# Performance work log

Measured on AMD Instinct MI355X. Metric: run time of the kernel, lower is better.

Reference implementation:

```python
import jax, jax.numpy as jnp
import numpy as np

N, C, R, T, H, W = 2, 256, 8, 4, 32, 32
CK = C // R  # key channels = 32


def setup_inputs() -> dict:
    key = jax.random.key(0)
    ks = jax.random.split(key, 10)
    s = 0.05  # small init so dual softmax is not saturated
    return {
        "x1": jax.random.normal(ks[0], (N, C, T, H, W), jnp.float32),
        "x2": jax.random.normal(ks[1], (N, C, T, H, W), jnp.float32),
        "Wk1": jax.random.normal(ks[2], (CK, C), jnp.float32) * s,
        "bk1": jax.random.normal(ks[3], (CK,), jnp.float32) * s,
        "Wk2": jax.random.normal(ks[4], (CK, C), jnp.float32) * s,
        "bk2": jax.random.normal(ks[5], (CK,), jnp.float32) * s,
        "Wv1": jax.random.normal(ks[6], (C, C), jnp.float32) * s,
        "bv1": jax.random.normal(ks[7], (C,), jnp.float32) * s,
        "Wv2": jax.random.normal(ks[8], (C, C), jnp.float32) * s,
        "bv2": jax.random.normal(ks[9], (C,), jnp.float32) * s,
    }


def reference(x1, x2, Wk1, bk1, Wk2, bk2, Wv1, bv1, Wv2, bv2):
    n, c, t, h, w = x1.shape
    L = t * h * w
    x1f = x1.reshape(n, c, L)  # [n, C, L]
    x2f = x2.reshape(n, c, L)
    # 1x1x1 Conv3d == per-position channel mixing
    k1 = jnp.einsum('kc,ncl->nkl', Wk1, x1f) + bk1[None, :, None]  # [n, CK, L]
    k2 = jnp.einsum('kc,ncl->nkl', Wk2, x2f) + bk2[None, :, None]
    v1 = jnp.einsum('dc,ncl->ndl', Wv1, x1f) + bv1[None, :, None]  # [n, C, L]
    v2 = jnp.einsum('dc,ncl->ndl', Wv2, x2f) + bv2[None, :, None]
    # cor[n, l, m] = sum_k k1[n,k,l] * k2[n,k,m]
    cor = jnp.einsum('nkl,nkm->nlm', k1, k2)  # [n, L, L]
    attn1 = jax.nn.softmax(cor, axis=2)  # rows normalized
    attn2 = jax.nn.softmax(cor, axis=1)  # cols normalized
    r1 = jnp.einsum('ncl,nlm->ncm', v1, attn1).reshape(n, c, t, h, w)
    r2 = jnp.einsum('ncm,nlm->ncl', v2, attn2).reshape(n, c, t, h, w)
    return (x1 + r1, x2 + r2)
```

## Files before the change

### kernel.cpp

```cpp
#include <hip/hip_runtime.h>
#include <hip/hip_bf16.h>

#define N_  2
#define C_  256
#define CK_ 32
#define L_  4096

typedef __attribute__((ext_vector_type(8))) short short8;
typedef __attribute__((ext_vector_type(4))) float f32x4;
typedef __attribute__((ext_vector_type(2))) unsigned int uint2v;
typedef unsigned short ushort;

__device__ __forceinline__ ushort f2bf(float f){
  unsigned u = __float_as_uint(f);
  u += 0x7fffu + ((u >> 16) & 1u);
  return (ushort)(u >> 16);
}

__device__ __forceinline__ f32x4 mfma16(short8 a, short8 b, f32x4 c){
  return __builtin_amdgcn_mfma_f32_16x16x32_bf16(a, b, c, 0, 0, 0);
}

__global__ __launch_bounds__(256) void convert_xw_kernel(
    const float* __restrict__ x1, const float* __restrict__ x2,
    ushort* __restrict__ xT1, ushort* __restrict__ xT2,
    const float* __restrict__ Wk1, const float* __restrict__ Wk2,
    const float* __restrict__ Wv1, const float* __restrict__ Wv2,
    ushort* __restrict__ o1, ushort* __restrict__ o2,
    ushort* __restrict__ o3, ushort* __restrict__ o4){
  int b = blockIdx.x, t = threadIdx.x;
  if (b >= 512){
    int idx = (b - 512) * 256 + t;
    const int KS = CK_ * C_;
    const int VS = C_ * C_;
    if (idx < KS)                 o1[idx] = f2bf(Wk1[idx]);
    else if (idx < 2*KS)          o2[idx - KS] = f2bf(Wk2[idx - KS]);
    else if (idx < 2*KS + VS)     o3[idx - 2*KS] = f2bf(Wv1[idx - 2*KS]);
    else if (idx < 2*KS + 2*VS)   o4[idx - 2*KS - VS] = f2bf(Wv2[idx - 2*KS - VS]);
    return;
  }
  __shared__ float tt[32][264];
  int z = b & 3; int n = z & 1;
  const float* x = (z >> 1) ? x2 : x1;
  ushort* xT = (z >> 1) ? xT2 : xT1;
  int tile = b >> 2;
  int l0 = (tile & 15) * 256, c0 = (tile >> 4) * 32;
  int w = t >> 6, lam = t & 63;
  const float* xs = x + (size_t)n * C_ * L_;
  ushort* xd = xT + (size_t)n * L_ * C_;
#pragma unroll
  for (int k = 0; k < 8; ++k){
    int cr = w * 8 + k;
    float4 f = *(const float4*)(xs + (size_t)(c0 + cr) * L_ + l0 + lam * 4);
    *(float4*)&tt[cr][lam * 4] = f;
  }
  __syncthreads();
  int g = t & 3, lr = t >> 2;
#pragma unroll
  for (int k = 0; k < 4; ++k){
    int l = k * 64 + lr;
    union { __hip_bfloat162 h[4]; short8 v; } pk;
#pragma unroll
    for (int j = 0; j < 4; ++j)
      pk.h[j] = __float22bfloat162_rn(
          make_float2(tt[g*8 + 2*j][l], tt[g*8 + 2*j + 1][l]));
    *(short8*)(xd + (size_t)(l0 + l) * C_ + c0 + g * 8) = pk.v;
  }
}

#define VP_OFF(nn, cc, pp) \
  ((((size_t)(nn)*128 + ((pp)>>5))*16 + ((cc)>>4))*512 + \
   (((pp)&31)>>3)*128 + ((cc)&15)*8 + ((pp)&7))

__global__ __launch_bounds__(256) void proj_kernel(
    const ushort* __restrict__ xT1, const ushort* __restrict__ xT2,
    const ushort* __restrict__ Wk1b, const ushort* __restrict__ Wk2b,
    const ushort* __restrict__ Wv1b, const ushort* __restrict__ Wv2b,
    const float* __restrict__ bk1, const float* __restrict__ bk2,
    const float* __restrict__ bv1, const float* __restrict__ bv2,
    ushort* __restrict__ k1t, ushort* __restrict__ k2t,
    ushort* __restrict__ v1,  ushort* __restrict__ v2){
  int bid = blockIdx.x;
  int n = bid & 1, side = (bid >> 1) & 1, jh = (bid >> 2) & 1, ltile = bid >> 3;
  const ushort* X  = side ? xT2 : xT1;
  const ushort* Wv = side ? Wv2b : Wv1b;
  const ushort* Wk = side ? Wk2b : Wk1b;
  const float*  bv = side ? bv2 : bv1;
  const float*  bk = side ? bk2 : bk1;
  ushort* vout = side ? v2 : v1;
  ushort* kout = side ? k2t : k1t;
  int l0 = ltile * 64;
  int t = threadIdx.x, w = t >> 6, lane = t & 63, quad = lane >> 4, low = lane & 15;
  __shared__ ushort xs[64][264];
  const ushort* Xn = X + ((size_t)n * L_ + l0) * C_;
#pragma unroll
  for (int i = 0; i < 8; ++i){
    int flat = i * 2048 + t * 8;
    *(short8*)&xs[flat >> 8][flat & 255] = *(const short8*)(Xn + flat);
  }
  __syncthreads();
  int lw = w * 16;
  int l = l0 + lw + low;
  int njt = jh ? 5 : 4;
  for (int u = 0; u < njt; ++u){
    int jt = jh ? (4 + u) : u;
    bool isK = (jt == 8);
    const ushort* W   = isK ? Wk : Wv + (size_t)jt * 32 * C_;
    const float* bias = isK ? bk : bv + jt * 32;
    f32x4 acc0 = {}, acc1 = {};
#pragma unroll
    for (int kc = 0; kc < 8; ++kc){
      short8 b  = *(const short8*)&xs[lw + low][kc*32 + quad*8];
      short8 a0 = *(const short8*)(W + (size_t)low * C_ + kc*32 + quad*8);
      short8 a1 = *(const short8*)(W + (size_t)(16 + low) * C_ + kc*32 + quad*8);
      acc0 = mfma16(a0, b, acc0);
      acc1 = mfma16(a1, b, acc1);
    }
#pragma unroll
    for (int js = 0; js < 2; ++js){
      f32x4 acc = js ? acc1 : acc0;
      f32x4 bb = *(const f32x4*)(bias + js*16 + quad*4);
      if (!isK){
#pragma unroll
        for (int r = 0; r < 4; ++r){
          int c = jt*32 + js*16 + quad*4 + r;
          vout[VP_OFF(n, c, l)] = f2bf(acc[r] + bb[r]);
        }
      } else {
        union { ushort u4[4]; uint2v vv_; } pk;
#pragma unroll
        for (int r = 0; r < 4; ++r) pk.u4[r] = f2bf(acc[r] + bb[r]);
        *(uint2v*)(kout + ((size_t)n*L_ + l)*CK_ + js*16 + quad*4) = pk.vv_;
      }
    }
  }
}

__global__ __launch_bounds__(256) void stats_kernel(
    const ushort* __restrict__ k1t, const ushort* __restrict__ k2t,
    float* __restrict__ S1part, float* __restrict__ S2part){
  int n = blockIdx.z;
  int m0 = blockIdx.x * 128, l0 = blockIdx.y * 128;
  int t = threadIdx.x, w = t >> 6, lane = t & 63, quad = lane >> 4, low = lane & 15;
  __shared__ float rowsum[128];
  __shared__ float colsum[4][128];
  const ushort* ka = k1t + (size_t)n * L_ * CK_;
  const ushort* kb = k2t + (size_t)n * L_ * CK_;
  short8 a[2], b[8];
#pragma unroll
  for (int lt = 0; lt < 2; ++lt)
    a[lt] = *(const short8*)(ka + (size_t)(l0 + w*32 + lt*16 + low)*CK_ + quad*8);
#pragma unroll
  for (int mt = 0; mt < 8; ++mt)
    b[mt] = *(const short8*)(kb + (size_t)(m0 + mt*16 + low)*CK_ + quad*8);
  float rp[2][4] = {}; float cp[8] = {};
  const f32x4 zero = {0.f, 0.f, 0.f, 0.f};
#pragma unroll
  for (int lt = 0; lt < 2; ++lt)
#pragma unroll
    for (int mt = 0; mt < 8; ++mt){
      f32x4 e = mfma16(a[lt], b[mt], zero);
#pragma unroll
      for (int r = 0; r < 4; ++r){
        float v = __builtin_amdgcn_exp2f(e[r] * 1.44269504088896f);
        rp[lt][r] += v;
        cp[mt] += v;
      }
    }
#pragma unroll
  for (int lt = 0; lt < 2; ++lt)
#pragma unroll
    for (int r = 0; r < 4; ++r){
      float v = rp[lt][r];
      v += __shfl_xor(v, 1); v += __shfl_xor(v, 2);
      v += __shfl_xor(v, 4); v += __shfl_xor(v, 8);
      if (low == 0) rowsum[w*32 + lt*16 + quad*4 + r] = v;
    }
#pragma unroll
  for (int mt = 0; mt < 8; ++mt){
    float v = cp[mt];
    v += __shfl_xor(v, 16); v += __shfl_xor(v, 32);
    if (quad == 0) colsum[w][mt*16 + low] = v;
  }
  __syncthreads();
  if (t < 128)
    S1part[((size_t)n*32 + blockIdx.x)*L_ + l0 + t] = rowsum[t];
  else {
    int m = t - 128;
    S2part[((size_t)n*32 + blockIdx.y)*L_ + m0 + m] =
        colsum[0][m] + colsum[1][m] + colsum[2][m] + colsum[3][m];
  }
}

__global__ __launch_bounds__(256) void reduce_inv_kernel(
    const float* __restrict__ S1part, const float* __restrict__ S2part,
    float* __restrict__ invS1, float* __restrict__ invS2){
  int idx = blockIdx.x * 256 + threadIdx.x;
  int which = idx >> 13;
  int r = idx & 8191;
  int n = r >> 12, l = r & 4095;
  const float* P = which ? S2part : S1part;
  float s = 0.f;
#pragma unroll
  for (int j = 0; j < 32; ++j) s += P[((size_t)n*32 + j)*L_ + l];
  (which ? invS2 : invS1)[(size_t)n*L_ + l] = -__builtin_amdgcn_logf(s);
}

#define LOG2E_ 1.44269504088896f

__global__ __launch_bounds__(256, 2) void cross_attn_r_kernel(
    const ushort* __restrict__ k1t, const ushort* __restrict__ k2t,
    const ushort* __restrict__ v1,  const ushort* __restrict__ v2,
    const float* __restrict__ invS1, const float* __restrict__ invS2,
    const float* __restrict__ x1, const float* __restrict__ x2,
    float* __restrict__ out){
  int bid = blockIdx.x;
  int slice = bid & 7;
  int qb = bid >> 3;
  int n = slice & 1;
  int which = (slice >> 1) & 1;
  int chalf = slice >> 2;
  const ushort* kA = which ? k2t : k1t;
  const ushort* kB = which ? k1t : k2t;
  const ushort* V  = which ? v2  : v1;
  const float* iS  = which ? invS2 : invS1;
  const float* X   = which ? x2 : x1;
  float* O = out + (size_t)which * N_ * C_ * L_;
  int q0 = qb * 64, c0 = chalf * 128;
  int t = threadIdx.x, w = t >> 6, lane = t & 63, quad = lane >> 4, low = lane & 15;
  __shared__ __align__(16) float red[4][16][68];
  const ushort* kAn = kA + (size_t)n * L_ * CK_;
  const ushort* kBn = kB + (size_t)n * L_ * CK_;
  const float*  iSn = iS + (size_t)n * L_;

  const ushort* kA_base = kAn + (size_t)((low >> 2) * 8 + (low & 3)) * CK_ + quad * 8;
  const float*  sv_base = iSn + quad * 8;
  const ushort* Vp_lane = V + ((size_t)n * 128 * 16 + chalf * 8) * 512 + (size_t)lane * 8;

  short8 be[4];
#pragma unroll
  for (int qs = 0; qs < 4; ++qs)
    be[qs] = *(const short8*)(kBn + (size_t)(q0 + qs*16 + low) * CK_ + quad * 8);

  f32x4 acc[8][4] = {};
  const f32x4 zero = {0.f, 0.f, 0.f, 0.f};

  int pfirst = w * 32;
  short8 a0 = *(const short8*)(kA_base + (size_t)pfirst * CK_);
  short8 a1 = *(const short8*)(kA_base + (size_t)(pfirst + 4) * CK_);
  f32x4 sv0 = *(const f32x4*)(sv_base + pfirst);
  f32x4 sv1 = *(const f32x4*)(sv_base + pfirst + 4);

  short8 vv[8];
  {
    const ushort* vt0 = Vp_lane + (size_t)w * 16 * 512;
#pragma unroll
    for (int ct = 0; ct < 8; ++ct)
      vv[ct] = *(const short8*)(vt0 + ct * 512);
  }

#define EPH(PB, QS) do{                                                        \
    f32x4 e0 = mfma16(a0, be[QS], zero);                                       \
    f32x4 e1 = mfma16(a1, be[QS], zero);                                       \
    float p0 = __builtin_amdgcn_exp2f(__fmaf_rn(e0[0], LOG2E_, sv0[0]));       \
    float p1 = __builtin_amdgcn_exp2f(__fmaf_rn(e0[1], LOG2E_, sv0[1]));       \
    float p2 = __builtin_amdgcn_exp2f(__fmaf_rn(e0[2], LOG2E_, sv0[2]));       \
    float p3 = __builtin_amdgcn_exp2f(__fmaf_rn(e0[3], LOG2E_, sv0[3]));       \
    float p4 = __builtin_amdgcn_exp2f(__fmaf_rn(e1[0], LOG2E_, sv1[0]));       \
    float p5 = __builtin_amdgcn_exp2f(__fmaf_rn(e1[1], LOG2E_, sv1[1]));       \
    float p6 = __builtin_amdgcn_exp2f(__fmaf_rn(e1[2], LOG2E_, sv1[2]));       \
    float p7 = __builtin_amdgcn_exp2f(__fmaf_rn(e1[3], LOG2E_, sv1[3]));       \
    union { __hip_bfloat162 h[4]; short8 v; } pk;                              \
    pk.h[0] = __float22bfloat162_rn(make_float2(p0, p1));                      \
    pk.h[1] = __float22bfloat162_rn(make_float2(p2, p3));                      \
    pk.h[2] = __float22bfloat162_rn(make_float2(p4, p5));                      \
    pk.h[3] = __float22bfloat162_rn(make_float2(p6, p7));                      \
    PB = pk.v;                                                                 \
  }while(0)

  for (int kk = 0; kk < L_ / 256; ++kk){
#pragma unroll
    for (int half = 0; half < 2; ++half){
      int it = 2*kk + half;
      int itn = (it + 1) & 31;
      const ushort* vt_next = Vp_lane + (size_t)(itn*4 + w) * 16 * 512;
      int pn = itn * 128 + w * 32;
      short8 pb0, pb1;
      EPH(pb0, 0);
      EPH(pb1, 1);
      __builtin_amdgcn_s_setprio(1);
#pragma unroll
      for (int ct = 0; ct < 8; ++ct){
        acc[ct][0] = mfma16(vv[ct], pb0, acc[ct][0]);
        acc[ct][1] = mfma16(vv[ct], pb1, acc[ct][1]);
      }
      __builtin_amdgcn_s_setprio(0);
      EPH(pb0, 2);
      EPH(pb1, 3);
      a0 = *(const short8*)(kA_base + (size_t)pn * CK_);
      a1 = *(const short8*)(kA_base + (size_t)(pn + 4) * CK_);
      sv0 = *(const f32x4*)(sv_base + pn);
      sv1 = *(const f32x4*)(sv_base + pn + 4);
      __builtin_amdgcn_s_setprio(1);
#pragma unroll
      for (int ct = 0; ct < 8; ++ct){
        acc[ct][2] = mfma16(vv[ct], pb0, acc[ct][2]);
        acc[ct][3] = mfma16(vv[ct], pb1, acc[ct][3]);
        vv[ct] = *(const short8*)(vt_next + ct * 512);
      }
      __builtin_amdgcn_s_setprio(0);
    }
  }
#undef EPH

  int cl = t >> 4, qg = (t & 15) * 4;
#pragma unroll
  for (int ct = 0; ct < 8; ++ct){
#pragma unroll
    for (int qs = 0; qs < 4; ++qs)
#pragma unroll
      for (int r = 0; r < 4; ++r)
        red[w][quad*4 + r][qs*16 + low] = acc[ct][qs][r];
    __syncthreads();
    f32x4 s0 = *(const f32x4*)&red[0][cl][qg];
    f32x4 s1 = *(const f32x4*)&red[1][cl][qg];
    f32x4 s2 = *(const f32x4*)&red[2][cl][qg];
    f32x4 s3 = *(const f32x4*)&red[3][cl][qg];
    f32x4 s = (s0 + s1) + (s2 + s3);
    size_t idx = ((size_t)n * C_ + c0 + ct*16 + cl) * L_ + q0 + qg;
    const float4 xv = *(const float4*)(X + idx);
    float4 o = make_float4(xv.x + s[0], xv.y + s[1], xv.z + s[2], xv.w + s[3]);
    *(float4*)(O + idx) = o;
    __syncthreads();
  }
}

extern "C" void kernel_launch(void* const* d_in, const int* in_sizes, int n_in,
                              void* d_out, int out_size, void* d_ws, size_t ws_size,
                              hipStream_t stream) {
  const float* x1  = (const float*)d_in[0];
  const float* x2  = (const float*)d_in[1];
  const float* Wk1 = (const float*)d_in[2];
  const float* bk1 = (const float*)d_in[3];
  const float* Wk2 = (const float*)d_in[4];
  const float* bk2 = (const float*)d_in[5];
  const float* Wv1 = (const float*)d_in[6];
  const float* bv1 = (const float*)d_in[7];
  const float* Wv2 = (const float*)d_in[8];
  const float* bv2 = (const float*)d_in[9];

  char* ws = (char*)d_ws;
  size_t off = 0;
  auto carve = [&](size_t bytes) -> void* {
    void* p = ws + off; off += (bytes + 255) & ~(size_t)255; return p;
  };
  ushort* xT1   = (ushort*)carve((size_t)N_*L_*C_*2);
  ushort* xT2   = (ushort*)carve((size_t)N_*L_*C_*2);
  ushort* Wk1b  = (ushort*)carve((size_t)CK_*C_*2);
  ushort* Wk2b  = (ushort*)carve((size_t)CK_*C_*2);
  ushort* Wv1b  = (ushort*)carve((size_t)C_*C_*2);
  ushort* Wv2b  = (ushort*)carve((size_t)C_*C_*2);
  ushort* k1t   = (ushort*)carve((size_t)N_*L_*CK_*2);
  ushort* k2t   = (ushort*)carve((size_t)N_*L_*CK_*2);
  ushort* v1    = (ushort*)carve((size_t)N_*C_*L_*2);
  ushort* v2    = (ushort*)carve((size_t)N_*C_*L_*2);
  float*  S1p   = (float*)carve((size_t)N_*32*L_*4);
  float*  S2p   = (float*)carve((size_t)N_*32*L_*4);
  float*  invS1 = (float*)carve((size_t)N_*L_*4);
  float*  invS2 = (float*)carve((size_t)N_*L_*4);

  convert_xw_kernel<<<dim3(512 + (2*CK_*C_ + 2*C_*C_) / 256), 256, 0, stream>>>(
      x1, x2, xT1, xT2, Wk1, Wk2, Wv1, Wv2, Wk1b, Wk2b, Wv1b, Wv2b);
  proj_kernel<<<dim3(512), 256, 0, stream>>>(
      xT1, xT2, Wk1b, Wk2b, Wv1b, Wv2b, bk1, bk2, bv1, bv2, k1t, k2t, v1, v2);
  stats_kernel<<<dim3(L_/128, L_/128, N_), 256, 0, stream>>>(k1t, k2t, S1p, S2p);
  reduce_inv_kernel<<<dim3(2*N_*L_/256), 256, 0, stream>>>(S1p, S2p, invS1, invS2);
  cross_attn_r_kernel<<<dim3(2 * N_ * (C_/128) * (L_/64), 1, 1), 256, 0, stream>>>(
      k1t, k2t, v1, v2, invS1, invS2, x1, x2, (float*)d_out);
}
```

Before: 169.4 us.

## Fuse partial-sum reduction into stats kernel via last-block atomic counters

Removes the separate reduce_inv kernel launch. The stats kernel now bumps per-row-strip and per-column-strip atomic counters, and the last block to finish each strip sums the 32 partials and writes the negative log normaliser. The counters are zeroed in the convert kernel. The epilogue of the cross-attention kernel is also changed from float4 accesses with per-thread column groups to scalar per-lane row stores, which alters coalescing and the LDS read pattern. The cost is extra fences and atomics in every stats block.

```diff
diff --git a/kernel.cpp b/kernel.cpp
--- a/kernel.cpp
+++ b/kernel.cpp
@@ -27,10 +27,12 @@
     const float* __restrict__ Wk1, const float* __restrict__ Wk2,
     const float* __restrict__ Wv1, const float* __restrict__ Wv2,
     ushort* __restrict__ o1, ushort* __restrict__ o2,
-    ushort* __restrict__ o3, ushort* __restrict__ o4){
+    ushort* __restrict__ o3, ushort* __restrict__ o4,
+    int* __restrict__ cnts){
   int b = blockIdx.x, t = threadIdx.x;
   if (b >= 512){
     int idx = (b - 512) * 256 + t;
+    if (b == 512 && t < 128) cnts[t] = 0;
     const int KS = CK_ * C_;
     const int VS = C_ * C_;
     if (idx < KS)                 o1[idx] = f2bf(Wk1[idx]);
@@ -138,12 +140,15 @@
 
 __global__ __launch_bounds__(256) void stats_kernel(
     const ushort* __restrict__ k1t, const ushort* __restrict__ k2t,
-    float* __restrict__ S1part, float* __restrict__ S2part){
+    float* __restrict__ S1part, float* __restrict__ S2part,
+    float* __restrict__ invS1, float* __restrict__ invS2,
+    int* __restrict__ cnts){
   int n = blockIdx.z;
   int m0 = blockIdx.x * 128, l0 = blockIdx.y * 128;
   int t = threadIdx.x, w = t >> 6, lane = t & 63, quad = lane >> 4, low = lane & 15;
   __shared__ float rowsum[128];
   __shared__ float colsum[4][128];
+  __shared__ int lastv[2];
   const ushort* ka = k1t + (size_t)n * L_ * CK_;
   const ushort* kb = k2t + (size_t)n * L_ * CK_;
   short8 a[2], b[8];
@@ -190,20 +195,25 @@
     S2part[((size_t)n*32 + blockIdx.y)*L_ + m0 + m] =
         colsum[0][m] + colsum[1][m] + colsum[2][m] + colsum[3][m];
   }
-}
-
-__global__ __launch_bounds__(256) void reduce_inv_kernel(
-    const float* __restrict__ S1part, const float* __restrict__ S2part,
-    float* __restrict__ invS1, float* __restrict__ invS2){
-  int idx = blockIdx.x * 256 + threadIdx.x;
-  int which = idx >> 13;
-  int r = idx & 8191;
-  int n = r >> 12, l = r & 4095;
-  const float* P = which ? S2part : S1part;
-  float s = 0.f;
-#pragma unroll
-  for (int j = 0; j < 32; ++j) s += P[((size_t)n*32 + j)*L_ + l];
-  (which ? invS2 : invS1)[(size_t)n*L_ + l] = -__builtin_amdgcn_logf(s);
+  __threadfence();
+  if (t == 0) lastv[0] = atomicAdd(&cnts[n*32 + blockIdx.y], 1);
+  if (t == 1) lastv[1] = atomicAdd(&cnts[64 + n*32 + blockIdx.x], 1);
+  __syncthreads();
+  if (lastv[0] == 31 && t < 128){
+    __threadfence();
+    float s = 0.f;
+#pragma unroll
+    for (int j = 0; j < 32; ++j) s += S1part[((size_t)n*32 + j)*L_ + l0 + t];
+    invS1[(size_t)n*L_ + l0 + t] = -__builtin_amdgcn_logf(s);
+  }
+  if (lastv[1] == 31 && t >= 128){
+    __threadfence();
+    int m = t - 128;
+    float s = 0.f;
+#pragma unroll
+    for (int j = 0; j < 32; ++j) s += S2part[((size_t)n*32 + j)*L_ + m0 + m];
+    invS2[(size_t)n*L_ + m0 + m] = -__builtin_amdgcn_logf(s);
+  }
 }
 
 #define LOG2E_ 1.44269504088896f
@@ -313,7 +323,6 @@
   }
 #undef EPH
 
-  int cl = t >> 4, qg = (t & 15) * 4;
 #pragma unroll
   for (int ct = 0; ct < 8; ++ct){
 #pragma unroll
@@ -322,15 +331,14 @@
       for (int r = 0; r < 4; ++r)
         red[w][quad*4 + r][qs*16 + low] = acc[ct][qs][r];
     __syncthreads();
-    f32x4 s0 = *(const f32x4*)&red[0][cl][qg];
-    f32x4 s1 = *(const f32x4*)&red[1][cl][qg];
-    f32x4 s2 = *(const f32x4*)&red[2][cl][qg];
-    f32x4 s3 = *(const f32x4*)&red[3][cl][qg];
-    f32x4 s = (s0 + s1) + (s2 + s3);
-    size_t idx = ((size_t)n * C_ + c0 + ct*16 + cl) * L_ + q0 + qg;
-    const float4 xv = *(const float4*)(X + idx);
-    float4 o = make_float4(xv.x + s[0], xv.y + s[1], xv.z + s[2], xv.w + s[3]);
-    *(float4*)(O + idx) = o;
+#pragma unroll
+    for (int k = 0; k < 4; ++k){
+      int row = k * 4 + w;
+      float s = (red[0][row][lane] + red[1][row][lane])
+              + (red[2][row][lane] + red[3][row][lane]);
+      size_t idx = ((size_t)n * C_ + c0 + ct*16 + row) * L_ + q0 + lane;
+      O[idx] = X[idx] + s;
+    }
     __syncthreads();
   }
 }
@@ -368,13 +376,14 @@
   float*  S2p   = (float*)carve((size_t)N_*32*L_*4);
   float*  invS1 = (float*)carve((size_t)N_*L_*4);
   float*  invS2 = (float*)carve((size_t)N_*L_*4);
+  int*    cnts  = (int*)carve(128 * 4);
 
   convert_xw_kernel<<<dim3(512 + (2*CK_*C_ + 2*C_*C_) / 256), 256, 0, stream>>>(
-      x1, x2, xT1, xT2, Wk1, Wk2, Wv1, Wv2, Wk1b, Wk2b, Wv1b, Wv2b);
+      x1, x2, xT1, xT2, Wk1, Wk2, Wv1, Wv2, Wk1b, Wk2b, Wv1b, Wv2b, cnts);
   proj_kernel<<<dim3(512), 256, 0, stream>>>(
       xT1, xT2, Wk1b, Wk2b, Wv1b, Wv2b, bk1, bk2, bv1, bv2, k1t, k2t, v1, v2);
-  stats_kernel<<<dim3(L_/128, L_/128, N_), 256, 0, stream>>>(k1t, k2t, S1p, S2p);
-  reduce_inv_kernel<<<dim3(2*N_*L_/256), 256, 0, stream>>>(S1p, S2p, invS1, invS2);
+  stats_kernel<<<dim3(L_/128, L_/128, N_), 256, 0, stream>>>(
+      k1t, k2t, S1p, S2p, invS1, invS2, cnts);
   cross_attn_r_kernel<<<dim3(2 * N_ * (C_/128) * (L_/64), 1, 1), 256, 0, stream>>>(
       k1t, k2t, v1, v2, invS1, invS2, x1, x2, (float*)d_out);
 }
```

Result: slower. 310.8 us (+83.4%).
